# Kernel optimization log

Hardware: AMD Instinct MI355X
Metric: run time of the kernel (lower is better)

Reference implementation:

```python
import jax, jax.numpy as jnp
import numpy as np

N_ITEMS = 50001   # n_items + 1 (padding row 0)
DIM = 256         # item_embedding_dim == hidden_size
PURPOSES = 3
TAU = 0.1
SEQ_LEN = 50
BATCH = 128
EPS = 0.01
STDV = 1.0 / np.sqrt(DIM)


def setup_inputs() -> dict:
    key = jax.random.key(0)
    ks = jax.random.split(key, 7)
    u = lambda k, s: jax.random.uniform(k, s, jnp.float32, -STDV, STDV)
    emb = u(ks[0], (N_ITEMS, DIM)).at[0].set(0.0)  # padding_idx=0
    emb_purpose = u(ks[1], (PURPOSES, DIM))
    w_ih = u(ks[2], (PURPOSES, 3 * DIM, DIM))
    w_hh = u(ks[3], (PURPOSES, 3 * DIM, DIM))
    b_ih = u(ks[4], (PURPOSES, 3 * DIM))
    b_hh = u(ks[5], (PURPOSES, 3 * DIM))
    seq = jax.random.randint(ks[6], (SEQ_LEN, BATCH), 0, N_ITEMS)
    return {"seq": seq, "emb": emb, "emb_purpose": emb_purpose,
            "w_ih": w_ih, "w_hh": w_hh, "b_ih": b_ih, "b_hh": b_hh}


def _psru(w_ih, w_hh, b_ih, b_hh, seq_embs, concen):
    # seq_embs: [B,S,D], concen: [B,S] -> final hidden [B,D]
    B = seq_embs.shape[0]
    H = w_hh.shape[1]

    def cell(h, xs):
        x, c = xs  # x: [B,D], c: [B]
        gi = x @ w_ih.T + b_ih
        gh = h @ w_hh.T + b_hh
        i_r, i_i, i_n = jnp.split(gi, 3, axis=1)
        h_r, h_i, h_n = jnp.split(gh, 3, axis=1)
        resetgate = jax.nn.sigmoid(i_r + h_r)
        inputgate = jax.nn.sigmoid(i_i + h_i)
        newgate = jnp.tanh(i_n + resetgate * h_n)
        cf = jnp.where(c >= EPS, c, 0.0)[:, None]  # concen gating
        hy = h - cf * inputgate * (h - newgate)
        return hy, None

    h0 = jnp.zeros((B, H), seq_embs.dtype)
    hN, _ = jax.lax.scan(cell, h0, (jnp.swapaxes(seq_embs, 0, 1), concen.T))
    return hN


def reference(seq, emb, emb_purpose, w_ih, w_hh, b_ih, b_hh):
    s = seq.T                               # [B,S]
    mask = (s != 0).astype(emb.dtype)       # padding mask
    seq_embs = emb[s]                       # [B,S,D]
    concen_score = jnp.einsum('bsd,pd->bsp', seq_embs, emb_purpose)
    concen_w = jax.nn.softmax(concen_score / TAU, axis=2) * mask[:, :, None]
    # run one PSRU per purpose, batched with vmap over the purpose axis
    hn = jax.vmap(_psru, in_axes=(0, 0, 0, 0, None, 2))(
        w_ih, w_hh, b_ih, b_hh, seq_embs, concen_w)   # [P,B,D]
    # target = arange(n_items) -> pos_embs = full embedding table
    tcw = jax.nn.softmax(emb @ emb_purpose.T, axis=1)  # [T,P]
    # scores[b,t] = sum_p tcw[t,p] * <hn[p,b,:], emb[t,:]>
    scores = jnp.einsum('pbd,td,tp->bt', hn, emb, tcw)  # [B,T]
    return scores
```

## Files before the change

### kernel.cpp

```cpp
#include <hip/hip_runtime.h>
#include <hip/hip_bf16.h>

#define S_LEN 50
#define BATCH 128
#define DIM 256
#define NITEMS 50001
#define NPAD 50048
#define GDIM 768
#define NSEQ 6400

typedef __attribute__((ext_vector_type(8))) short short8;
typedef __attribute__((ext_vector_type(4))) short short4_;
typedef __attribute__((ext_vector_type(4))) float float4_;

static __device__ __forceinline__ unsigned short f2bf(float x){
  union { float f; unsigned u; } v; v.f = x;
  unsigned r = v.u + 0x7FFFu + ((v.u >> 16) & 1u);
  return (unsigned short)(r >> 16);
}
static __device__ __forceinline__ float bf2f(unsigned short h){
  union { unsigned u; float f; } v; v.u = ((unsigned)h) << 16;
  return v.f;
}
static __device__ __forceinline__ float rcpf_(float x){ return __builtin_amdgcn_rcpf(x); }
static __device__ __forceinline__ float exp2f_(float x){ return __builtin_amdgcn_exp2f(x); }

__global__ __launch_bounds__(256) void k_prep(
        const float* __restrict__ wih, unsigned short* __restrict__ wihT,
        const float* __restrict__ emb, const float* __restrict__ embp,
        const int* __restrict__ seq, unsigned short* __restrict__ xT,
        float* __restrict__ cfb){
  __shared__ unsigned short sT[8192];
  int bid = blockIdx.x;
  int tid = threadIdx.x;
  int w = tid >> 6, lane = tid & 63;
  int r16 = w*4 + (lane >> 4);
  int c0  = lane & 15;
  if (bid < 144){
    const float4_* er = (const float4_*)(wih + (size_t)(bid*16 + r16)*DIM);
    #pragma unroll
    for (int k=0;k<4;k++){
      float4_ v = er[k*16 + c0];
      short4_ o;
      #pragma unroll
      for (int jj=0;jj<4;jj++) o[jj] = (short)f2bf(v[jj]);
      int di = k*64 + c0*4;
      int kf = di >> 5, qd = (di >> 3) & 3, j = di & 7;
      *(short4_*)(sT + (kf*64 + r16 + qd*16)*8 + j) = o;
    }
    __syncthreads();
    unsigned short* dst = wihT + (size_t)bid*4096 + tid*16;
    *(short8*)(dst)     = *(const short8*)(sT + tid*16);
    *(short8*)(dst + 8) = *(const short8*)(sT + tid*16 + 8);
    return;
  }
  {
    int bx = bid - 144;
    int wid = bx*16 + r16;
    int s = wid >> 7, b = wid & 127;
    int item = seq[s*BATCH + b];
    const float4_* er = (const float4_*)(emb + (size_t)item*DIM);
    const float4_* pp = (const float4_*)embp;
    float d0=0.f, d1=0.f, d2=0.f;
    #pragma unroll
    for (int k=0;k<4;k++){
      float4_ v = er[k*16 + c0];
      short4_ o;
      #pragma unroll
      for (int jj=0;jj<4;jj++) o[jj] = (short)f2bf(v[jj]);
      int di = k*64 + c0*4;
      int kf = di >> 5, qd = (di >> 3) & 3, j = di & 7;
      *(short4_*)(sT + (kf*64 + r16 + qd*16)*8 + j) = o;
      float4_ e0 = pp[k*16 + c0], e1 = pp[64 + k*16 + c0], e2 = pp[128 + k*16 + c0];
      #pragma unroll
      for (int jj=0;jj<4;jj++){ d0 += v[jj]*e0[jj]; d1 += v[jj]*e1[jj]; d2 += v[jj]*e2[jj]; }
    }
    #pragma unroll
    for (int off=1; off<16; off<<=1){
      d0 += __shfl_xor(d0,off); d1 += __shfl_xor(d1,off); d2 += __shfl_xor(d2,off);
    }
    if (c0 == 0){
      float m = fmaxf(d0, fmaxf(d1,d2));
      float a0 = __expf((d0-m)*10.f), a1 = __expf((d1-m)*10.f), a2 = __expf((d2-m)*10.f);
      float inv = (item != 0) ? rcpf_(a0+a1+a2) : 0.f;
      float cc0 = a0*inv, cc1 = a1*inv, cc2 = a2*inv;
      cfb[wid]          = (cc0 >= 0.01f) ? cc0 : 0.f;
      cfb[NSEQ + wid]   = (cc1 >= 0.01f) ? cc1 : 0.f;
      cfb[2*NSEQ + wid] = (cc2 >= 0.01f) ? cc2 : 0.f;
    }
    __syncthreads();
    unsigned short* dst = xT + (size_t)bx*4096 + tid*16;
    *(short8*)(dst)     = *(const short8*)(sT + tid*16);
    *(short8*)(dst + 8) = *(const short8*)(sT + tid*16 + 8);
  }
}

__global__ __launch_bounds__(256) void k_gi(const unsigned short* __restrict__ xT,
        const unsigned short* __restrict__ wihT, const float* __restrict__ bih,
        const float* __restrict__ bhh, unsigned short* __restrict__ gi2,
        const float* __restrict__ whh, unsigned short* __restrict__ whh_bf){
  int bid = blockIdx.x;
  int tid = threadIdx.x;
  if (bid >= 3600){
    int i = (bid - 3600)*256 + tid;
    float4_ y = ((const float4_*)whh)[i];
    short4_ v;
    #pragma unroll
    for (int j=0;j<4;j++) v[j] = (short)f2bf(y[j]);
    ((short4_*)whh_bf)[i] = v;
    return;
  }
  int nx  = bid % 12;
  int rem = bid / 12;
  int yy  = rem % 100;
  int p   = rem / 100;
  int wv = tid >> 6;
  int lane = tid & 63;
  int col = lane & 15, q = lane >> 4;
  int mt = yy*4 + wv;
  float4_ z4 = {0.f,0.f,0.f,0.f};
  float4_ acc[4];
  #pragma unroll
  for (int t=0;t<4;t++) acc[t] = z4;
  #pragma unroll
  for (int kf=0; kf<8; kf++){
    short8 a = *(const short8*)(xT + (((size_t)mt*8 + kf)*64 + lane)*8);
    #pragma unroll
    for (int t=0;t<4;t++){
      short8 bb = *(const short8*)(wihT + (((size_t)(p*48 + nx*4 + t)*8 + kf)*64 + lane)*8);
      acc[t] = __builtin_amdgcn_mfma_f32_16x16x32_bf16(a, bb, acc[t], 0, 0, 0);
    }
  }
  int s     = yy >> 1;
  int slice = (yy & 1)*4 + wv;
  size_t X = (size_t)(p*S_LEN + s)*8 + slice;
  int g = nx >> 2;
  #pragma unroll
  for (int t=0;t<4;t++){
    int nn = nx*4 + t;
    int wc = (nn >> 1) & 7;
    int tt = nn & 1;
    int n  = nn*16 + col;
    float bv = bih[p*GDIM + n] + ((g < 2) ? bhh[p*GDIM + n] : 0.f);
    short4_ ov;
    #pragma unroll
    for (int i=0;i<4;i++) ov[i] = (short)f2bf(acc[t][i] + bv);
    *(short4_*)(gi2 + X*12288 + (size_t)(g*16 + wc*2 + tt)*256 + lane*4) = ov;
  }
}

__global__ __launch_bounds__(512) __attribute__((amdgpu_waves_per_eu(2, 2)))
void k_rnn(const unsigned short* __restrict__ whh_bf,
         const unsigned short* __restrict__ gi2, const float* __restrict__ bhh,
         const float* __restrict__ cfb, unsigned short* __restrict__ hnT,
         const float* __restrict__ emb, const float* __restrict__ embp,
         unsigned short* __restrict__ embT, float* __restrict__ tcw){
  extern __shared__ char lds[];
  int bid = blockIdx.x;
  int tid = threadIdx.x;
  if (bid >= 24){
    int sub = tid >> 8;
    int t2  = tid & 255;
    unsigned short* sT = (unsigned short*)lds + sub*8192;
    int w = t2 >> 6, lane = t2 & 63;
    int r16 = w*4 + (lane >> 4);
    int c0  = lane & 15;
    int bx2 = (bid - 24)*2 + sub;
    int row = bx2*16 + r16;
    bool valid = row < NITEMS;
    const float4_* er = (const float4_*)(emb + (size_t)row*DIM);
    const float4_* pp = (const float4_*)embp;
    float d0=0.f, d1=0.f, d2=0.f;
    #pragma unroll
    for (int k=0;k<4;k++){
      float4_ v = valid ? er[k*16 + c0] : float4_{0.f,0.f,0.f,0.f};
      short4_ o;
      #pragma unroll
      for (int jj=0;jj<4;jj++) o[jj] = (short)f2bf(v[jj]);
      int di = k*64 + c0*4;
      int kf = di >> 5, qd = (di >> 3) & 3, j = di & 7;
      *(short4_*)(sT + (kf*64 + r16 + qd*16)*8 + j) = o;
      float4_ e0 = pp[k*16 + c0], e1 = pp[64 + k*16 + c0], e2 = pp[128 + k*16 + c0];
      #pragma unroll
      for (int jj=0;jj<4;jj++){ d0 += v[jj]*e0[jj]; d1 += v[jj]*e1[jj]; d2 += v[jj]*e2[jj]; }
    }
    #pragma unroll
    for (int off=1; off<16; off<<=1){
      d0 += __shfl_xor(d0,off); d1 += __shfl_xor(d1,off); d2 += __shfl_xor(d2,off);
    }
    if (c0 == 0 && valid){
      float m = fmaxf(d0, fmaxf(d1,d2));
      float a0 = __expf(d0-m), a1 = __expf(d1-m), a2 = __expf(d2-m);
      float inv = rcpf_(a0+a1+a2);
      tcw[row*3+0] = a0*inv; tcw[row*3+1] = a1*inv; tcw[row*3+2] = a2*inv;
    }
    __syncthreads();
    unsigned short* dst = embT + (size_t)bx2*4096 + t2*16;
    *(short8*)(dst)     = *(const short8*)(sT + t2*16);
    *(short8*)(dst + 8) = *(const short8*)(sT + t2*16 + 8);
    return;
  }
  float* cfs = (float*)(lds + 147456);
  int p  = bid >> 3;
  int slice = bid & 7;
  int b0 = slice * 16;
  int w = tid >> 6, lane = tid & 63;
  int col = lane & 15;
  int q = lane >> 4;
  int kq = q * 8;
  const unsigned short* Wp = whh_bf + (size_t)p*GDIM*DIM;

  for (int i = tid; i < 8192; i += 512) ((unsigned short*)lds)[i] = 0;
  for (int i = tid; i < 800; i += 512) cfs[i] = cfb[p*NSEQ + (i>>4)*BATCH + b0 + (i&15)];
  {
    const unsigned short* Wn = Wp + (size_t)512*DIM;
    #pragma unroll
    for (int r = 0; r < 16; r++){
      int j = r*512 + tid;
      int kf = j >> 10, row = (j >> 2) & 255, qs = j & 3;
      short8 v = *(const short8*)(Wn + (size_t)row*DIM + kf*32 + ((qs ^ ((row>>1)&3)) << 3));
      *(short8*)(lds + 16384 + j*16) = v;
    }
  }

  float bias_n0 = bhh[p*GDIM + 512 + w*32 + col];
  float bias_n1 = bhh[p*GDIM + 512 + w*32 + 16 + col];

  short8 Bf[8][4];
  #pragma unroll
  for (int kf=0; kf<8; kf++){
    #pragma unroll
    for (int t=0;t<4;t++){
      int gc = (t>>1)*256 + w*32 + (t&1)*16 + col;
      Bf[kf][t] = *(const short8*)(Wp + ((size_t)gc << 8) + kf*32 + kq);
      asm volatile("" : "+a"(Bf[kf][t]));
    }
  }
  const char* wn0 = lds + 16384 + (size_t)(w*32 + col)*64 + ((q ^ ((col>>1)&3)) << 4);
  const char* wn1 = wn0 + 16*64;
  int swz  = (lane & 7) << 4;
  float hreg[2][4];
  #pragma unroll
  for (int t=0;t<2;t++){
    #pragma unroll
    for (int i=0;i<4;i++) hreg[t][i] = 0.f;
  }
  const size_t GSTRIDE = (size_t)8*12288;
  const unsigned short* gbase =
      gi2 + ((size_t)p*S_LEN*8 + slice)*12288 + (size_t)(w*2)*256 + lane*4;
  short4_ cur[6], nxt[6];
  #pragma unroll
  for (int t=0;t<6;t++)
    cur[t] = *(const short4_*)(gbase + (t>>1)*4096 + (t&1)*256);
  __syncthreads();

  const float K1 = -1.442695041f;
  const float K2 =  2.885390082f;
  float4_ z4 = {0.f,0.f,0.f,0.f};
  for (int s = 0; s < S_LEN; s++){
    int rbuf = s & 1, wbuf = rbuf ^ 1;
    int sn = (s+1 < S_LEN) ? s+1 : 0;
    const unsigned short* gnp = gbase + (size_t)sn*GSTRIDE;
    #pragma unroll
    for (int t=0;t<6;t++)
      nxt[t] = *(const short4_*)(gnp + (t>>1)*4096 + (t&1)*256);
    float4_ acc[6];
    #pragma unroll
    for (int t=0;t<6;t++) acc[t] = z4;
    const char* hrow = lds + rbuf*8192 + col*512;
    #pragma unroll
    for (int kf=0; kf<8; kf++){
      int ko = (kf*64 + q*16);
      short8 a = *(const short8*)(hrow + (ko ^ swz));
      #pragma unroll
      for (int t=0;t<4;t++)
        acc[t] = __builtin_amdgcn_mfma_f32_16x16x32_bf16(a, Bf[kf][t], acc[t], 0, 0, 0);
      short8 b4 = *(const short8*)(wn0 + kf*16384);
      acc[4] = __builtin_amdgcn_mfma_f32_16x16x32_bf16(a, b4, acc[4], 0, 0, 0);
      short8 b5 = *(const short8*)(wn1 + kf*16384);
      acc[5] = __builtin_amdgcn_mfma_f32_16x16x32_bf16(a, b5, acc[5], 0, 0, 0);
    }
    float4_ cfv = *(const float4_*)(cfs + s*16 + 4*q);
    char* wbase = lds + wbuf*8192;
    int d0b = 2*(w*32 + col);
    #pragma unroll
    for (int i=0;i<4;i++){
      int rb = 4*q + i;
      float hy01[2];
      #pragma unroll
      for (int t=0;t<2;t++){
        float bn = t ? bias_n1 : bias_n0;
        float r = rcpf_(1.f + exp2f_(K1*(bf2f((unsigned short)cur[t][i])   + acc[t][i])));
        float z = rcpf_(1.f + exp2f_(K1*(bf2f((unsigned short)cur[2+t][i]) + acc[2+t][i])));
        float pre = bf2f((unsigned short)cur[4+t][i]) + r*(acc[4+t][i] + bn);
        float n = 1.f - 2.f*rcpf_(exp2f_(K2*pre) + 1.f);
        float ho = hreg[t][i];
        float hy = ho - cfv[i]*z*(ho - n);
        hreg[t][i] = hy;
        hy01[t] = hy;
      }
      unsigned pk;
      asm("v_cvt_pk_bf16_f32 %0, %1, %2" : "=v"(pk) : "v"(hy01[0]), "v"(hy01[1]));
      char* rowp = wbase + rb*512;
      int sw = (rb & 7) << 4;
      *(unsigned short*)(rowp + (d0b ^ sw))        = (unsigned short)pk;
      *(unsigned short*)(rowp + ((d0b + 32) ^ sw)) = (unsigned short)(pk >> 16);
    }
    #pragma unroll
    for (int t=0;t<6;t++) cur[t] = nxt[t];
    __syncthreads();
  }
  #pragma unroll
  for (int t=0; t<2; t++){
    int d  = w*32 + t*16 + col;
    int kf = d >> 5;
    int qd = (d >> 3) & 3;
    int j  = d & 7;
    #pragma unroll
    for (int i=0; i<4; i++){
      int rb = 4*q + i;
      hnT[(((size_t)p*8 + slice)*8 + kf)*512 + (size_t)(rb + qd*16)*8 + j] = f2bf(hreg[t][i]);
    }
  }
}

__global__ __launch_bounds__(256) void k_score(const unsigned short* __restrict__ embT,
        const unsigned short* __restrict__ hnT, const float* __restrict__ tcw,
        float* __restrict__ out){
  __shared__ float sm[64*129];
  int w = threadIdx.x >> 6, lane = threadIdx.x & 63;
  int col = lane & 15, q = lane >> 4;
  int t16 = blockIdx.x*4 + w;
  int trow = t16*16 + col;
  float4_ z4 = {0.f,0.f,0.f,0.f};
  float4_ acc[3][8];
  #pragma unroll
  for (int p=0;p<3;p++){
    #pragma unroll
    for (int m=0;m<8;m++) acc[p][m] = z4;
  }
  #pragma unroll
  for (int kf=0; kf<8; kf++){
    short8 bb = *(const short8*)(embT + (((size_t)t16*8 + kf)*64 + lane)*8);
    #pragma unroll
    for (int p=0;p<3;p++){
      #pragma unroll
      for (int m=0;m<8;m++){
        short8 a = *(const short8*)(hnT + ((((size_t)p*8 + m)*8 + kf)*512) + lane*8);
        acc[p][m] = __builtin_amdgcn_mfma_f32_16x16x32_bf16(a, bb, acc[p][m], 0, 0, 0);
      }
    }
  }
  float w0=0.f, w1=0.f, w2=0.f;
  if (trow < NITEMS){ w0 = tcw[trow*3+0]; w1 = tcw[trow*3+1]; w2 = tcw[trow*3+2]; }
  #pragma unroll
  for (int m=0;m<8;m++){
    #pragma unroll
    for (int i=0;i<4;i++){
      sm[(w*16 + col)*129 + m*16 + 4*q + i] =
          w0*acc[0][m][i] + w1*acc[1][m][i] + w2*acc[2][m][i];
    }
  }
  __syncthreads();
  int trowW = blockIdx.x*64 + lane;
  if (trowW < NITEMS){
    float* orow = out + trowW;
    #pragma unroll 4
    for (int c=0; c<32; c++){
      int b = w*32 + c;
      orow[(size_t)b*NITEMS] = sm[lane*129 + b];
    }
  }
}

extern "C" void kernel_launch(void* const* d_in, const int* in_sizes, int n_in,
                              void* d_out, int out_size, void* d_ws, size_t ws_size,
                              hipStream_t stream) {
  const int*   seq  = (const int*)d_in[0];
  const float* emb  = (const float*)d_in[1];
  const float* embp = (const float*)d_in[2];
  const float* wih  = (const float*)d_in[3];
  const float* whh  = (const float*)d_in[4];
  const float* bih  = (const float*)d_in[5];
  const float* bhh  = (const float*)d_in[6];
  float* out = (float*)d_out;

  char* ws = (char*)d_ws;
  size_t off = 0;
  auto alloc = [&](size_t bytes) -> void* {
    void* r = ws + off; off += (bytes + 255) & ~(size_t)255; return r;
  };
  unsigned short* embT   = (unsigned short*)alloc((size_t)NPAD*DIM*2);
  unsigned short* xT     = (unsigned short*)alloc((size_t)NSEQ*DIM*2);
  unsigned short* wihT   = (unsigned short*)alloc((size_t)3*GDIM*DIM*2);
  unsigned short* whh_bf = (unsigned short*)alloc((size_t)3*GDIM*DIM*2);
  unsigned short* gi2    = (unsigned short*)alloc((size_t)3*NSEQ*GDIM*2);
  float* tcw = (float*)alloc((size_t)NITEMS*3*4);
  float* cfb = (float*)alloc((size_t)3*NSEQ*4);
  unsigned short* hnT = (unsigned short*)alloc((size_t)3*BATCH*DIM*2);

  k_prep<<<544, 256, 0, stream>>>(wih, wihT, emb, embp, seq, xT, cfb);
  k_gi<<<4176, 256, 0, stream>>>(xT, wihT, bih, bhh, gi2, whh, whh_bf);

  (void)hipFuncSetAttribute((const void*)k_rnn,
        hipFuncAttributeMaxDynamicSharedMemorySize, 150656);
  k_rnn<<<1588, 512, 150656, stream>>>(whh_bf, gi2, bhh, cfb, hnT,
                                       emb, embp, embT, tcw);

  k_score<<<NPAD/64, 256, 0, stream>>>(embT, hnT, tcw, out);
}
```

Before: 182.8 us.

## Stage W_ih tiles in LDS in input-gate GEMM and move W_hh conversion to prep

The input-projection GEMM now gives each block 8 N-tiles instead of 4, so the grid shrinks from 3600 to 1800 blocks. Each block first copies a 64KB slice of the bf16 W_ih into LDS, and all four waves read B fragments from there instead of from global memory. The W_hh fp32-to-bf16 conversion blocks move from k_gi into k_prep. The change cuts redundant global weight reads and block count, but adds a serial LDS fill and a barrier, and uses more LDS per block, which may lower occupancy.

```diff
diff --git a/kernel.cpp b/kernel.cpp
--- a/kernel.cpp
+++ b/kernel.cpp
@@ -27,17 +27,28 @@
 
 __global__ __launch_bounds__(256) void k_prep(
         const float* __restrict__ wih, unsigned short* __restrict__ wihT,
+        const float* __restrict__ whh, unsigned short* __restrict__ whh_bf,
         const float* __restrict__ emb, const float* __restrict__ embp,
         const int* __restrict__ seq, unsigned short* __restrict__ xT,
         float* __restrict__ cfb){
   __shared__ unsigned short sT[8192];
   int bid = blockIdx.x;
   int tid = threadIdx.x;
+  if (bid < 576){
+    int i = bid*256 + tid;
+    float4_ y = ((const float4_*)whh)[i];
+    short4_ v;
+    #pragma unroll
+    for (int j=0;j<4;j++) v[j] = (short)f2bf(y[j]);
+    ((short4_*)whh_bf)[i] = v;
+    return;
+  }
   int w = tid >> 6, lane = tid & 63;
   int r16 = w*4 + (lane >> 4);
   int c0  = lane & 15;
-  if (bid < 144){
-    const float4_* er = (const float4_*)(wih + (size_t)(bid*16 + r16)*DIM);
+  if (bid < 720){
+    int bx = bid - 576;
+    const float4_* er = (const float4_*)(wih + (size_t)(bx*16 + r16)*DIM);
     #pragma unroll
     for (int k=0;k<4;k++){
       float4_ v = er[k*16 + c0];
@@ -49,13 +60,13 @@
       *(short4_*)(sT + (kf*64 + r16 + qd*16)*8 + j) = o;
     }
     __syncthreads();
-    unsigned short* dst = wihT + (size_t)bid*4096 + tid*16;
+    unsigned short* dst = wihT + (size_t)bx*4096 + tid*16;
     *(short8*)(dst)     = *(const short8*)(sT + tid*16);
     *(short8*)(dst + 8) = *(const short8*)(sT + tid*16 + 8);
     return;
   }
   {
-    int bx = bid - 144;
+    int bx = bid - 720;
     int wid = bx*16 + r16;
     int s = wid >> 7, b = wid & 127;
     int item = seq[s*BATCH + b];
@@ -97,54 +108,52 @@
 
 __global__ __launch_bounds__(256) void k_gi(const unsigned short* __restrict__ xT,
         const unsigned short* __restrict__ wihT, const float* __restrict__ bih,
-        const float* __restrict__ bhh, unsigned short* __restrict__ gi2,
-        const float* __restrict__ whh, unsigned short* __restrict__ whh_bf){
+        const float* __restrict__ bhh, unsigned short* __restrict__ gi2){
+  extern __shared__ unsigned short sB[];
   int bid = blockIdx.x;
   int tid = threadIdx.x;
-  if (bid >= 3600){
-    int i = (bid - 3600)*256 + tid;
-    float4_ y = ((const float4_*)whh)[i];
-    short4_ v;
-    #pragma unroll
-    for (int j=0;j<4;j++) v[j] = (short)f2bf(y[j]);
-    ((short4_*)whh_bf)[i] = v;
-    return;
-  }
-  int nx  = bid % 12;
-  int rem = bid / 12;
+  int nb  = bid % 6;
+  int rem = bid / 6;
   int yy  = rem % 100;
   int p   = rem / 100;
+  const unsigned short* Bsrc = wihT + (size_t)(p*48 + nb*8)*4096;
+  #pragma unroll
+  for (int r = 0; r < 16; r++){
+    int c16 = r*256 + tid;
+    *(short8*)(sB + c16*8) = *(const short8*)(Bsrc + c16*8);
+  }
+  __syncthreads();
   int wv = tid >> 6;
   int lane = tid & 63;
   int col = lane & 15, q = lane >> 4;
   int mt = yy*4 + wv;
   float4_ z4 = {0.f,0.f,0.f,0.f};
-  float4_ acc[4];
-  #pragma unroll
-  for (int t=0;t<4;t++) acc[t] = z4;
+  float4_ acc[8];
+  #pragma unroll
+  for (int t=0;t<8;t++) acc[t] = z4;
   #pragma unroll
   for (int kf=0; kf<8; kf++){
     short8 a = *(const short8*)(xT + (((size_t)mt*8 + kf)*64 + lane)*8);
     #pragma unroll
-    for (int t=0;t<4;t++){
-      short8 bb = *(const short8*)(wihT + (((size_t)(p*48 + nx*4 + t)*8 + kf)*64 + lane)*8);
-      acc[t] = __builtin_amdgcn_mfma_f32_16x16x32_bf16(a, bb, acc[t], 0, 0, 0);
+    for (int nt=0; nt<8; nt++){
+      short8 bb = *(const short8*)(sB + ((nt*8 + kf)*64 + lane)*8);
+      acc[nt] = __builtin_amdgcn_mfma_f32_16x16x32_bf16(a, bb, acc[nt], 0, 0, 0);
     }
   }
   int s     = yy >> 1;
   int slice = (yy & 1)*4 + wv;
   size_t X = (size_t)(p*S_LEN + s)*8 + slice;
-  int g = nx >> 2;
-  #pragma unroll
-  for (int t=0;t<4;t++){
-    int nn = nx*4 + t;
+  int g = (nb*8) >> 4;
+  #pragma unroll
+  for (int nt=0; nt<8; nt++){
+    int nn = nb*8 + nt;
     int wc = (nn >> 1) & 7;
     int tt = nn & 1;
     int n  = nn*16 + col;
     float bv = bih[p*GDIM + n] + ((g < 2) ? bhh[p*GDIM + n] : 0.f);
     short4_ ov;
     #pragma unroll
-    for (int i=0;i<4;i++) ov[i] = (short)f2bf(acc[t][i] + bv);
+    for (int i=0;i<4;i++) ov[i] = (short)f2bf(acc[nt][i] + bv);
     *(short4_*)(gi2 + X*12288 + (size_t)(g*16 + wc*2 + tt)*256 + lane*4) = ov;
   }
 }
@@ -399,8 +408,11 @@
   float* cfb = (float*)alloc((size_t)3*NSEQ*4);
   unsigned short* hnT = (unsigned short*)alloc((size_t)3*BATCH*DIM*2);
 
-  k_prep<<<544, 256, 0, stream>>>(wih, wihT, emb, embp, seq, xT, cfb);
-  k_gi<<<4176, 256, 0, stream>>>(xT, wihT, bih, bhh, gi2, whh, whh_bf);
+  k_prep<<<1120, 256, 0, stream>>>(wih, wihT, whh, whh_bf, emb, embp, seq, xT, cfb);
+
+  (void)hipFuncSetAttribute((const void*)k_gi,
+        hipFuncAttributeMaxDynamicSharedMemorySize, 65536);
+  k_gi<<<1800, 256, 65536, stream>>>(xT, wihT, bih, bhh, gi2);
 
   (void)hipFuncSetAttribute((const void*)k_rnn,
         hipFuncAttributeMaxDynamicSharedMemorySize, 150656);
```

New measurement: 181.6 us. Within noise of the previous version (-0.7%).
